# Optimization experiments

Measured on AMD Instinct MI355X. Metric: run time of the kernel, lower is better.

## Reference

```python
import jax, jax.numpy as jnp
import numpy as np

N_NODES = 50000
N_EDGES = 600000
H_DIM = 128
BN_EPS = 1e-5


def setup_inputs() -> dict:
    key = jax.random.key(0)
    k1, k2, k3, k4 = jax.random.split(key, 4)
    ent_emb = jax.random.normal(k1, (N_NODES, H_DIM), dtype=jnp.float32)
    # xavier_normal_ init for the 128x128 weight
    std = float(np.sqrt(2.0 / (H_DIM + H_DIM)))
    neigh_w = jax.random.normal(k2, (H_DIM, H_DIM), dtype=jnp.float32) * std
    gamma = jnp.ones((H_DIM,), dtype=jnp.float32)
    beta = jnp.zeros((H_DIM,), dtype=jnp.float32)
    src = jax.random.randint(k3, (N_EDGES,), 0, N_NODES, dtype=jnp.int32)
    dst = jax.random.randint(k4, (N_EDGES,), 0, N_NODES, dtype=jnp.int32)
    return {"ent_emb": ent_emb, "neigh_w": neigh_w, "gamma": gamma,
            "beta": beta, "src": src, "dst": dst}


def reference(ent_emb, neigh_w, gamma, beta, src, dst):
    # Edge dot-product scores: u_dot_v('emb','emb')  -> [E]
    e_src = ent_emb[src]                      # [E, H]
    e_dst = ent_emb[dst]                      # [E, H]
    scores = jnp.sum(e_src * e_dst, axis=-1)  # [E]

    # edge_softmax: softmax over incoming edges of each destination node
    seg_max = jax.ops.segment_max(scores, dst, num_segments=N_NODES)
    seg_max = jnp.where(jnp.isfinite(seg_max), seg_max, 0.0)  # nodes w/o edges
    e = jnp.exp(scores - seg_max[dst])                         # [E]
    seg_sum = jax.ops.segment_sum(e, dst, num_segments=N_NODES)
    norm = e / seg_sum[dst]                                    # [E]

    # update_all(u_mul_e, sum): weighted gather-sum aggregation
    msg = e_src * norm[:, None]                                # [E, H]
    neigh = jax.ops.segment_sum(msg, dst, num_segments=N_NODES)  # [N, H]

    # matmul + BatchNorm1d (training-mode batch stats) + tanh
    h = neigh @ neigh_w                                        # [N, H]
    mean = jnp.mean(h, axis=0)
    var = jnp.var(h, axis=0)  # biased, matches torch BN normalization
    h = (h - mean) * jax.lax.rsqrt(var + BN_EPS) * gamma + beta
    return jnp.tanh(h)
```

## Files before the change

kernel.cpp:

```cpp
#include <hip/hip_runtime.h>
#include <hip/hip_fp16.h>
#include <math.h>

#define N_NODES 50000
#define N_EDGES 600000
#define H 128
#define BN_EPS 1e-5f
#define MAXDEG 48
#define CNT_STRIDE 16

typedef unsigned short ushort_t;
typedef unsigned int uint_t;

template <int CTRL>
static __device__ __forceinline__ float dpp_xor_f(float x) {
    int xi = __builtin_bit_cast(int, x);
    int r = __builtin_amdgcn_update_dpp(0, xi, CTRL, 0xF, 0xF, true);
    return __builtin_bit_cast(float, r);
}
#define DPP_XOR1 0xB1
#define DPP_XOR2 0x4E
#define DPP_XOR8 0x128

static __device__ __forceinline__ float dot2f(uint_t au, uint_t bu, float c) {
#if __has_builtin(__builtin_amdgcn_fdot2)
    typedef _Float16 f16x2 __attribute__((ext_vector_type(2)));
    return __builtin_amdgcn_fdot2(__builtin_bit_cast(f16x2, au),
                                  __builtin_bit_cast(f16x2, bu), c, false);
#else
    __half2 a = __builtin_bit_cast(__half2, au);
    __half2 b = __builtin_bit_cast(__half2, bu);
    float2 af = __half22float2(a), bf = __half22float2(b);
    return c + af.x * bf.x + af.y * bf.y;
#endif
}

__global__ void k_scatter(const int* __restrict__ src, const int* __restrict__ dst,
                          int* __restrict__ cnt, ushort_t* __restrict__ slots,
                          const float* __restrict__ emb, __half* __restrict__ emb16,
                          const float* __restrict__ W, uint_t* __restrict__ w16p) {
    int i = blockIdx.x * blockDim.x + threadIdx.x;
    int e0 = i * 4;
    if (e0 < N_EDGES) {
        int4 s4 = *(const int4*)(src + e0);
        int4 d4 = *(const int4*)(dst + e0);
        int p0 = atomicAdd(cnt + d4.x * CNT_STRIDE, 1);
        int p1 = atomicAdd(cnt + d4.y * CNT_STRIDE, 1);
        int p2 = atomicAdd(cnt + d4.z * CNT_STRIDE, 1);
        int p3 = atomicAdd(cnt + d4.w * CNT_STRIDE, 1);
        if (p0 < MAXDEG) slots[d4.x * MAXDEG + p0] = (ushort_t)s4.x;
        if (p1 < MAXDEG) slots[d4.y * MAXDEG + p1] = (ushort_t)s4.y;
        if (p2 < MAXDEG) slots[d4.z * MAXDEG + p2] = (ushort_t)s4.z;
        if (p3 < MAXDEG) slots[d4.w * MAXDEG + p3] = (ushort_t)s4.w;
    }
    if (i < N_NODES * H / 8) {
        float4 f0 = ((const float4*)emb)[2 * i];
        float4 f1 = ((const float4*)emb)[2 * i + 1];
        union { uint4 u; __half2 h2[4]; } U;
        U.h2[0] = __floats2half2_rn(f0.x, f0.y);
        U.h2[1] = __floats2half2_rn(f0.z, f0.w);
        U.h2[2] = __floats2half2_rn(f1.x, f1.y);
        U.h2[3] = __floats2half2_rn(f1.z, f1.w);
        ((uint4*)emb16)[i] = U.u;
    }
    if (i < H * H / 8) {
        int e  = 4 * i;
        int k2 = e >> 7;
        int j  = e & 127;
        float4 w0 = *(const float4*)(W + (size_t)(2 * k2) * H + j);
        float4 w1 = *(const float4*)(W + (size_t)(2 * k2 + 1) * H + j);
        union { uint4 u; __half2 h2[4]; } U;
        U.h2[0] = __floats2half2_rn(w0.x, w1.x);
        U.h2[1] = __floats2half2_rn(w0.y, w1.y);
        U.h2[2] = __floats2half2_rn(w0.z, w1.z);
        U.h2[3] = __floats2half2_rn(w0.w, w1.w);
        ((uint4*)w16p)[i] = U.u;
    }
}

#define F4SCALE(a, s) { (a).x *= (s); (a).y *= (s); (a).z *= (s); (a).w *= (s); }
#define F4FMA(a, e, v) { (a).x += (e)*(v).x; (a).y += (e)*(v).y; (a).z += (e)*(v).z; (a).w += (e)*(v).w; }
#define F4DPPADD8(a) { (a).x += dpp_xor_f<DPP_XOR8>((a).x); (a).y += dpp_xor_f<DPP_XOR8>((a).y); \
                       (a).z += dpp_xor_f<DPP_XOR8>((a).z); (a).w += dpp_xor_f<DPP_XOR8>((a).w); }
#define F4SHFLADD(a, msk) { (a).x += __shfl_xor((a).x, msk, 64); (a).y += __shfl_xor((a).y, msk, 64); \
                            (a).z += __shfl_xor((a).z, msk, 64); (a).w += __shfl_xor((a).w, msk, 64); }

__global__ __launch_bounds__(256) void k_fused(const float* __restrict__ emb,
                                               const __half* __restrict__ emb16,
                                               const int* __restrict__ cnt,
                                               const ushort_t* __restrict__ slots,
                                               __half* __restrict__ neigh) {
    int wid = (blockIdx.x * blockDim.x + threadIdx.x) >> 6;
    int lane = threadIdx.x & 63;
    if (wid >= N_NODES) return;
    int g = lane >> 3;
    int l = lane & 7;

    int deg = min(cnt[wid * CNT_STRIDE], MAXDEG);
    int sid = slots[wid * MAXDEG + min(lane, MAXDEG - 1)];

    const float4* rd = (const float4*)(emb + (size_t)wid * H) + l * 4;
    float4 b0 = rd[0], b1 = rd[1], b2 = rd[2], b3 = rd[3];

    float m = -INFINITY, ssum = 0.0f;
    float4 acc0 = {0,0,0,0}, acc1 = {0,0,0,0}, acc2 = {0,0,0,0}, acc3 = {0,0,0,0};

    for (int cb = 0; cb < deg; cb += 8) {
        int e = cb + g;
        bool valid = e < deg;
        int s = __shfl(sid, valid ? e : 0, 64);
        const uint4* rs = (const uint4*)(emb16 + (size_t)s * H) + l * 2;
        uint4 p0 = rs[0], p1 = rs[1];
        const __half2* h0 = (const __half2*)&p0;
        const __half2* h1 = (const __half2*)&p1;
        float2 t0 = __half22float2(h0[0]), t1 = __half22float2(h0[1]);
        float2 t2 = __half22float2(h0[2]), t3 = __half22float2(h0[3]);
        float2 t4 = __half22float2(h1[0]), t5 = __half22float2(h1[1]);
        float2 t6 = __half22float2(h1[2]), t7 = __half22float2(h1[3]);
        float4 a0 = make_float4(t0.x, t0.y, t1.x, t1.y);
        float4 a1 = make_float4(t2.x, t2.y, t3.x, t3.y);
        float4 a2 = make_float4(t4.x, t4.y, t5.x, t5.y);
        float4 a3 = make_float4(t6.x, t6.y, t7.x, t7.y);

        float v = a0.x*b0.x + a0.y*b0.y + a0.z*b0.z + a0.w*b0.w
                + a1.x*b1.x + a1.y*b1.y + a1.z*b1.z + a1.w*b1.w
                + a2.x*b2.x + a2.y*b2.y + a2.z*b2.z + a2.w*b2.w
                + a3.x*b3.x + a3.y*b3.y + a3.z*b3.z + a3.w*b3.w;
        v += dpp_xor_f<DPP_XOR1>(v);
        v += dpp_xor_f<DPP_XOR2>(v);
        v += __shfl_xor(v, 4, 64);
        if (!valid) v = -INFINITY;

        float cmax = v;
        cmax = fmaxf(cmax, dpp_xor_f<DPP_XOR8>(cmax));
        cmax = fmaxf(cmax, __shfl_xor(cmax, 16, 64));
        cmax = fmaxf(cmax, __shfl_xor(cmax, 32, 64));
        float mnew = fmaxf(m, cmax);
        if (mnew > m) {
            float scale = __expf(m - mnew);
            ssum *= scale;
            F4SCALE(acc0, scale); F4SCALE(acc1, scale);
            F4SCALE(acc2, scale); F4SCALE(acc3, scale);
            m = mnew;
        }

        float ev = __expf(v - m);
        ssum += ev;
        F4FMA(acc0, ev, a0); F4FMA(acc1, ev, a1);
        F4FMA(acc2, ev, a2); F4FMA(acc3, ev, a3);
    }

    ssum += dpp_xor_f<DPP_XOR8>(ssum);
    ssum += __shfl_xor(ssum, 16, 64);
    ssum += __shfl_xor(ssum, 32, 64);
    F4DPPADD8(acc0);     F4DPPADD8(acc1);     F4DPPADD8(acc2);     F4DPPADD8(acc3);
    F4SHFLADD(acc0, 16); F4SHFLADD(acc1, 16); F4SHFLADD(acc2, 16); F4SHFLADD(acc3, 16);
    F4SHFLADD(acc0, 32); F4SHFLADD(acc1, 32); F4SHFLADD(acc2, 32); F4SHFLADD(acc3, 32);

    float inv = (deg > 0) ? 1.0f / ssum : 0.0f;
    if (g == 0) {
        F4SCALE(acc0, inv); F4SCALE(acc1, inv); F4SCALE(acc2, inv); F4SCALE(acc3, inv);
        union { uint4 u; __half2 h2[4]; } U0, U1;
        U0.h2[0] = __floats2half2_rn(acc0.x, acc0.y);
        U0.h2[1] = __floats2half2_rn(acc0.z, acc0.w);
        U0.h2[2] = __floats2half2_rn(acc1.x, acc1.y);
        U0.h2[3] = __floats2half2_rn(acc1.z, acc1.w);
        U1.h2[0] = __floats2half2_rn(acc2.x, acc2.y);
        U1.h2[1] = __floats2half2_rn(acc2.z, acc2.w);
        U1.h2[2] = __floats2half2_rn(acc3.x, acc3.y);
        U1.h2[3] = __floats2half2_rn(acc3.z, acc3.w);
        uint4* po = (uint4*)(neigh + (size_t)wid * H);
        po[2 * l] = U0.u;
        po[2 * l + 1] = U1.u;
    }
}

#define MM_ROWS 64
__global__ __launch_bounds__(256, 4) void k_matmul(const __half* __restrict__ neigh,
                                                   const uint_t* __restrict__ w16p,
                                                   __half* __restrict__ hout,
                                                   float* __restrict__ stats) {
    __shared__ uint_t Wl[(H / 2) * H];
    int t = threadIdx.x;
    int n0 = blockIdx.x * MM_ROWS;
    int cg = t & 15, rg = t >> 4;
    int j0 = cg * 8;
    int r0 = n0 + rg * 4;

    for (int idx = t; idx < H * H / 8; idx += 256)
        ((uint4*)Wl)[idx] = ((const uint4*)w16p)[idx];

    const __half* pr[4];
    bool valid[4];
#pragma unroll
    for (int i = 0; i < 4; ++i) {
        int n = r0 + i;
        valid[i] = (n < N_NODES);
        pr[i] = neigh + (size_t)(valid[i] ? n : 0) * H;
    }

    __syncthreads();

    float acc[4][8] = {};
    for (int k2 = 0; k2 < H / 2; k2 += 4) {
        uint4 rv[4];
#pragma unroll
        for (int i = 0; i < 4; ++i) rv[i] = *(const uint4*)(pr[i] + 2 * k2);
#pragma unroll
        for (int kk = 0; kk < 4; ++kk) {
            const uint4* wp = (const uint4*)&Wl[(k2 + kk) * H + j0];
            uint4 wA = wp[0];
            uint4 wB = wp[1];
#pragma unroll
            for (int i = 0; i < 4; ++i) {
                uint_t a = ((const uint_t*)&rv[i])[kk];
                acc[i][0] = dot2f(a, wA.x, acc[i][0]);
                acc[i][1] = dot2f(a, wA.y, acc[i][1]);
                acc[i][2] = dot2f(a, wA.z, acc[i][2]);
                acc[i][3] = dot2f(a, wA.w, acc[i][3]);
                acc[i][4] = dot2f(a, wB.x, acc[i][4]);
                acc[i][5] = dot2f(a, wB.y, acc[i][5]);
                acc[i][6] = dot2f(a, wB.z, acc[i][6]);
                acc[i][7] = dot2f(a, wB.w, acc[i][7]);
            }
        }
    }

#pragma unroll
    for (int i = 0; i < 4; ++i) {
        if (valid[i]) {
            union { uint4 u; __half2 h2[4]; } U;
            U.h2[0] = __floats2half2_rn(acc[i][0], acc[i][1]);
            U.h2[1] = __floats2half2_rn(acc[i][2], acc[i][3]);
            U.h2[2] = __floats2half2_rn(acc[i][4], acc[i][5]);
            U.h2[3] = __floats2half2_rn(acc[i][6], acc[i][7]);
            *(uint4*)(hout + (size_t)(r0 + i) * H + j0) = U.u;
        }
    }

    __syncthreads();
    float* Sl = (float*)Wl;
    float* Ql = (float*)Wl + 16 * H;
#pragma unroll
    for (int c = 0; c < 8; ++c) {
        float s = 0.0f, q = 0.0f;
#pragma unroll
        for (int i = 0; i < 4; ++i) {
            if (valid[i]) { s += acc[i][c]; q += acc[i][c] * acc[i][c]; }
        }
        Sl[rg * H + j0 + c] = s;
        Ql[rg * H + j0 + c] = q;
    }
    __syncthreads();
    if (t < H) {
        float s = 0.0f;
#pragma unroll
        for (int r = 0; r < 16; ++r) s += Sl[r * H + t];
        atomicAdd(stats + t, s);
    } else {
        int j = t - H;
        float q = 0.0f;
#pragma unroll
        for (int r = 0; r < 16; ++r) q += Ql[r * H + j];
        atomicAdd(stats + 128 + j, q);
    }
}

__device__ __forceinline__ float tanh_fast(float x) {
    float e = __expf(2.0f * x);
    return 1.0f - 2.0f / (e + 1.0f);
}

__global__ __launch_bounds__(256) void k_apply_f16(const __half* __restrict__ h,
                                                   float* __restrict__ out,
                                                   const float* __restrict__ stats,
                                                   const float* __restrict__ gamma,
                                                   const float* __restrict__ beta) {
    __shared__ float sc[128], sh[128];
    int t = threadIdx.x;
    if (t < 128) {
        float mean = stats[t] * (1.0f / N_NODES);
        float var = stats[128 + t] * (1.0f / N_NODES) - mean * mean;
        var = fmaxf(var, 0.0f);
        float s = gamma[t] * rsqrtf(var + BN_EPS);
        sc[t] = s;
        sh[t] = beta[t] - mean * s;
    }
    __syncthreads();
    int i = blockIdx.x * 256 + t;
    if (i < N_NODES * H / 8) {
        union { uint4 u; __half2 h2[4]; } U;
        U.u = ((const uint4*)h)[i];
        int jb = (i & 15) * 8;
        float2 f0 = __half22float2(U.h2[0]);
        float2 f1 = __half22float2(U.h2[1]);
        float2 f2 = __half22float2(U.h2[2]);
        float2 f3 = __half22float2(U.h2[3]);
        float4 o0, o1;
        o0.x = tanh_fast(f0.x * sc[jb]     + sh[jb]);
        o0.y = tanh_fast(f0.y * sc[jb + 1] + sh[jb + 1]);
        o0.z = tanh_fast(f1.x * sc[jb + 2] + sh[jb + 2]);
        o0.w = tanh_fast(f1.y * sc[jb + 3] + sh[jb + 3]);
        o1.x = tanh_fast(f2.x * sc[jb + 4] + sh[jb + 4]);
        o1.y = tanh_fast(f2.y * sc[jb + 5] + sh[jb + 5]);
        o1.z = tanh_fast(f3.x * sc[jb + 6] + sh[jb + 6]);
        o1.w = tanh_fast(f3.y * sc[jb + 7] + sh[jb + 7]);
        ((float4*)out)[2 * i]     = o0;
        ((float4*)out)[2 * i + 1] = o1;
    }
}

extern "C" void kernel_launch(void* const* d_in, const int* in_sizes, int n_in,
                              void* d_out, int out_size, void* d_ws, size_t ws_size,
                              hipStream_t stream) {
    const float* emb   = (const float*)d_in[0];
    const float* W     = (const float*)d_in[1];
    const float* gamma = (const float*)d_in[2];
    const float* beta  = (const float*)d_in[3];
    const int*   src   = (const int*)d_in[4];
    const int*   dst   = (const int*)d_in[5];
    float* out = (float*)d_out;

    int*      cnt   = (int*)d_ws;
    float*    stats = (float*)(cnt + (size_t)N_NODES * CNT_STRIDE);
    ushort_t* slots = (ushort_t*)((int*)(stats + 256) + 4);
    __half*   neigh = (__half*)(slots + (size_t)N_NODES * MAXDEG);
    __half*   hbuf  = neigh + (size_t)N_NODES * H;
    __half*   emb16 = hbuf + (size_t)N_NODES * H;
    uint_t*   w16p  = (uint_t*)(emb16 + (size_t)N_NODES * H);

    hipMemsetAsync(cnt, 0, ((size_t)N_NODES * CNT_STRIDE + 260) * sizeof(int), stream);
    int nthr_sc = N_NODES * H / 8;
    k_scatter<<<(nthr_sc + 255) / 256, 256, 0, stream>>>(src, dst, cnt, slots, emb, emb16, W, w16p);
    k_fused<<<(N_NODES * 64 + 255) / 256, 256, 0, stream>>>(emb, emb16, cnt, slots, neigh);
    int nblk_mm = (N_NODES + MM_ROWS - 1) / MM_ROWS;
    k_matmul<<<nblk_mm, 256, 0, stream>>>(neigh, w16p, hbuf, stats);
    k_apply_f16<<<(N_NODES * H / 8 + 255) / 256, 256, 0, stream>>>(hbuf, out, stats, gamma, beta);
}
```

Baseline: 195.7 us.

## Replace fdot2 matmul with MFMA 16x16x32 f16 and padded transposed weights

Rewrites the node-feature x weight matmul to use MFMA 16x16x32 f16 instructions instead of per-thread packed fdot2 FMAs. The weight is now pre-transposed into a padded [128][136] half layout so each lane can read its B fragment from LDS with less bank conflict. Each wave computes a 16-row by 128-column tile across 8 accumulators, and the batch-norm partial stats are rebuilt from the MFMA output layout. Output stores become scalar half writes, which are less coalesced than the old 16-byte stores.

```diff
diff --git a/kernel.cpp b/kernel.cpp
--- a/kernel.cpp
+++ b/kernel.cpp
@@ -11,6 +11,8 @@
 
 typedef unsigned short ushort_t;
 typedef unsigned int uint_t;
+typedef _Float16 f16x8 __attribute__((ext_vector_type(8)));
+typedef float f32x4 __attribute__((ext_vector_type(4)));
 
 template <int CTRL>
 static __device__ __forceinline__ float dpp_xor_f(float x) {
@@ -22,23 +24,12 @@
 #define DPP_XOR2 0x4E
 #define DPP_XOR8 0x128
 
-static __device__ __forceinline__ float dot2f(uint_t au, uint_t bu, float c) {
-#if __has_builtin(__builtin_amdgcn_fdot2)
-    typedef _Float16 f16x2 __attribute__((ext_vector_type(2)));
-    return __builtin_amdgcn_fdot2(__builtin_bit_cast(f16x2, au),
-                                  __builtin_bit_cast(f16x2, bu), c, false);
-#else
-    __half2 a = __builtin_bit_cast(__half2, au);
-    __half2 b = __builtin_bit_cast(__half2, bu);
-    float2 af = __half22float2(a), bf = __half22float2(b);
-    return c + af.x * bf.x + af.y * bf.y;
-#endif
-}
+#define WT_STRIDE 136
 
 __global__ void k_scatter(const int* __restrict__ src, const int* __restrict__ dst,
                           int* __restrict__ cnt, ushort_t* __restrict__ slots,
                           const float* __restrict__ emb, __half* __restrict__ emb16,
-                          const float* __restrict__ W, uint_t* __restrict__ w16p) {
+                          const float* __restrict__ W, __half* __restrict__ wt) {
     int i = blockIdx.x * blockDim.x + threadIdx.x;
     int e0 = i * 4;
     if (e0 < N_EDGES) {
@@ -64,17 +55,16 @@
         ((uint4*)emb16)[i] = U.u;
     }
     if (i < H * H / 8) {
-        int e  = 4 * i;
-        int k2 = e >> 7;
-        int j  = e & 127;
-        float4 w0 = *(const float4*)(W + (size_t)(2 * k2) * H + j);
-        float4 w1 = *(const float4*)(W + (size_t)(2 * k2 + 1) * H + j);
+        int j  = i >> 4;
+        int kc = (i & 15) * 8;
         union { uint4 u; __half2 h2[4]; } U;
-        U.h2[0] = __floats2half2_rn(w0.x, w1.x);
-        U.h2[1] = __floats2half2_rn(w0.y, w1.y);
-        U.h2[2] = __floats2half2_rn(w0.z, w1.z);
-        U.h2[3] = __floats2half2_rn(w0.w, w1.w);
-        ((uint4*)w16p)[i] = U.u;
+#pragma unroll
+        for (int q = 0; q < 4; ++q) {
+            float lo = W[(size_t)(kc + 2 * q) * H + j];
+            float hi = W[(size_t)(kc + 2 * q + 1) * H + j];
+            U.h2[q] = __floats2half2_rn(lo, hi);
+        }
+        *(uint4*)(wt + (size_t)j * WT_STRIDE + kc) = U.u;
     }
 }
 
@@ -177,79 +167,69 @@
 
 #define MM_ROWS 64
 __global__ __launch_bounds__(256, 4) void k_matmul(const __half* __restrict__ neigh,
-                                                   const uint_t* __restrict__ w16p,
+                                                   const __half* __restrict__ wt,
                                                    __half* __restrict__ hout,
                                                    float* __restrict__ stats) {
-    __shared__ uint_t Wl[(H / 2) * H];
+    __shared__ __half Wl[H * WT_STRIDE];
     int t = threadIdx.x;
-    int n0 = blockIdx.x * MM_ROWS;
-    int cg = t & 15, rg = t >> 4;
-    int j0 = cg * 8;
-    int r0 = n0 + rg * 4;
-
-    for (int idx = t; idx < H * H / 8; idx += 256)
-        ((uint4*)Wl)[idx] = ((const uint4*)w16p)[idx];
-
-    const __half* pr[4];
-    bool valid[4];
-#pragma unroll
-    for (int i = 0; i < 4; ++i) {
-        int n = r0 + i;
-        valid[i] = (n < N_NODES);
-        pr[i] = neigh + (size_t)(valid[i] ? n : 0) * H;
-    }
+    int wv = t >> 6;
+    int l  = t & 63;
+    int r0 = blockIdx.x * MM_ROWS + wv * 16;
+
+    for (int idx = t; idx < H * WT_STRIDE / 8; idx += 256)
+        ((uint4*)Wl)[idx] = ((const uint4*)wt)[idx];
+
+    int rowA = r0 + (l & 15);
+    if (rowA >= N_NODES) rowA = 0;
+    const __half* pa = neigh + (size_t)rowA * H + ((l >> 4) * 4);
 
     __syncthreads();
 
-    float acc[4][8] = {};
-    for (int k2 = 0; k2 < H / 2; k2 += 4) {
-        uint4 rv[4];
-#pragma unroll
-        for (int i = 0; i < 4; ++i) rv[i] = *(const uint4*)(pr[i] + 2 * k2);
-#pragma unroll
-        for (int kk = 0; kk < 4; ++kk) {
-            const uint4* wp = (const uint4*)&Wl[(k2 + kk) * H + j0];
-            uint4 wA = wp[0];
-            uint4 wB = wp[1];
-#pragma unroll
-            for (int i = 0; i < 4; ++i) {
-                uint_t a = ((const uint_t*)&rv[i])[kk];
-                acc[i][0] = dot2f(a, wA.x, acc[i][0]);
-                acc[i][1] = dot2f(a, wA.y, acc[i][1]);
-                acc[i][2] = dot2f(a, wA.z, acc[i][2]);
-                acc[i][3] = dot2f(a, wA.w, acc[i][3]);
-                acc[i][4] = dot2f(a, wB.x, acc[i][4]);
-                acc[i][5] = dot2f(a, wB.y, acc[i][5]);
-                acc[i][6] = dot2f(a, wB.z, acc[i][6]);
-                acc[i][7] = dot2f(a, wB.w, acc[i][7]);
-            }
-        }
-    }
-
-#pragma unroll
-    for (int i = 0; i < 4; ++i) {
-        if (valid[i]) {
-            union { uint4 u; __half2 h2[4]; } U;
-            U.h2[0] = __floats2half2_rn(acc[i][0], acc[i][1]);
-            U.h2[1] = __floats2half2_rn(acc[i][2], acc[i][3]);
-            U.h2[2] = __floats2half2_rn(acc[i][4], acc[i][5]);
-            U.h2[3] = __floats2half2_rn(acc[i][6], acc[i][7]);
-            *(uint4*)(hout + (size_t)(r0 + i) * H + j0) = U.u;
+    f32x4 acc[8] = {};
+#pragma unroll
+    for (int kk = 0; kk < 4; ++kk) {
+        uint2 a_lo = *(const uint2*)(pa + kk * 32);
+        uint2 a_hi = *(const uint2*)(pa + kk * 32 + 16);
+        uint4 au = make_uint4(a_lo.x, a_lo.y, a_hi.x, a_hi.y);
+        f16x8 af = __builtin_bit_cast(f16x8, au);
+#pragma unroll
+        for (int jt = 0; jt < 8; ++jt) {
+            const __half* pb = Wl + (size_t)(jt * 16 + (l & 15)) * WT_STRIDE
+                             + kk * 32 + ((l >> 4) * 4);
+            uint2 b_lo = *(const uint2*)(pb);
+            uint2 b_hi = *(const uint2*)(pb + 16);
+            uint4 bu = make_uint4(b_lo.x, b_lo.y, b_hi.x, b_hi.y);
+            f16x8 bf = __builtin_bit_cast(f16x8, bu);
+            acc[jt] = __builtin_amdgcn_mfma_f32_16x16x32_f16(af, bf, acc[jt], 0, 0, 0);
+        }
+    }
+
+    int rbase = r0 + (l >> 4) * 4;
+#pragma unroll
+    for (int jt = 0; jt < 8; ++jt) {
+        int col = jt * 16 + (l & 15);
+#pragma unroll
+        for (int reg = 0; reg < 4; ++reg) {
+            int row = rbase + reg;
+            if (row < N_NODES)
+                hout[(size_t)row * H + col] = __float2half(acc[jt][reg]);
         }
     }
 
     __syncthreads();
     float* Sl = (float*)Wl;
-    float* Ql = (float*)Wl + 16 * H;
-#pragma unroll
-    for (int c = 0; c < 8; ++c) {
+    float* Ql = Sl + 16 * H;
+    int srow = wv * 4 + (l >> 4);
+#pragma unroll
+    for (int jt = 0; jt < 8; ++jt) {
+        int col = jt * 16 + (l & 15);
         float s = 0.0f, q = 0.0f;
 #pragma unroll
-        for (int i = 0; i < 4; ++i) {
-            if (valid[i]) { s += acc[i][c]; q += acc[i][c] * acc[i][c]; }
-        }
-        Sl[rg * H + j0 + c] = s;
-        Ql[rg * H + j0 + c] = q;
+        for (int reg = 0; reg < 4; ++reg) {
+            if (rbase + reg < N_NODES) { float v = acc[jt][reg]; s += v; q += v * v; }
+        }
+        Sl[srow * H + col] = s;
+        Ql[srow * H + col] = q;
     }
     __syncthreads();
     if (t < H) {
@@ -327,13 +307,13 @@
     __half*   neigh = (__half*)(slots + (size_t)N_NODES * MAXDEG);
     __half*   hbuf  = neigh + (size_t)N_NODES * H;
     __half*   emb16 = hbuf + (size_t)N_NODES * H;
-    uint_t*   w16p  = (uint_t*)(emb16 + (size_t)N_NODES * H);
+    __half*   wt    = emb16 + (size_t)N_NODES * H;
 
     hipMemsetAsync(cnt, 0, ((size_t)N_NODES * CNT_STRIDE + 260) * sizeof(int), stream);
     int nthr_sc = N_NODES * H / 8;
-    k_scatter<<<(nthr_sc + 255) / 256, 256, 0, stream>>>(src, dst, cnt, slots, emb, emb16, W, w16p);
+    k_scatter<<<(nthr_sc + 255) / 256, 256, 0, stream>>>(src, dst, cnt, slots, emb, emb16, W, wt);
     k_fused<<<(N_NODES * 64 + 255) / 256, 256, 0, stream>>>(emb, emb16, cnt, slots, neigh);
     int nblk_mm = (N_NODES + MM_ROWS - 1) / MM_ROWS;
-    k_matmul<<<nblk_mm, 256, 0, stream>>>(neigh, w16p, hbuf, stats);
+    k_matmul<<<nblk_mm, 256, 0, stream>>>(neigh, wt, hbuf, stats);
     k_apply_f16<<<(N_NODES * H / 8 + 255) / 256, 256, 0, stream>>>(hbuf, out, stats, gamma, beta);
 }
```

New measurement: 188.8 us, median of 2. -3.5%, faster.
